# Performance work log

Hardware: AMD Instinct MI355X
Metric: run time of the kernel (lower is better)

The kernel has to match this reference:

```python
import jax, jax.numpy as jnp
import numpy as np
from jax import lax

# db4 analysis filters (pywt convention)
DEC_LO = np.array([-0.010597401785069032, 0.0328830116668852, 0.030841381835560764,
                   -0.18703481171909309, -0.027983769416859854, 0.6308807679298589,
                   0.7148465705529157, 0.2303778133088965], dtype=np.float32)
DEC_HI = np.array([-0.2303778133088965, 0.7148465705529157, -0.6308807679298589,
                   -0.027983769416859854, 0.18703481171909309, 0.030841381835560764,
                   -0.0328830116668852, -0.010597401785069032], dtype=np.float32)
LF = 8          # db4 filter length
J = 4           # wavelet levels
H = 768         # hidden size per modality
B, S = 8, 2048  # batch, seq len

# pytorch_wavelets cross-correlates with time-reversed dec filters (afb)
H0R = jnp.asarray(DEC_LO[::-1].copy())
H1R = jnp.asarray(DEC_HI[::-1].copy())
# conv_transpose(rec) == cross-correlation with flip(rec); flip(rec)=dec
G0F = jnp.asarray(DEC_LO)
G1F = jnp.asarray(DEC_HI)


def afb1d(x):
    """One analysis level along last axis, zero-pad mode. x: (B, C, N)."""
    b, c, n = x.shape
    outsize = (n + LF - 1) // 2          # pywt.dwt_coeff_len, mode='zero'
    p = 2 * (outsize - 1) - n + LF       # total pad (extra goes on the right)
    kern = jnp.stack([H0R, H1R])[:, None, :]               # (2,1,LF)
    y = lax.conv_general_dilated(x.reshape(b * c, 1, n), kern,
                                 (2,), [(p // 2, p - p // 2)])
    return y[:, 0].reshape(b, c, outsize), y[:, 1].reshape(b, c, outsize)


def sfb1d(lo, hi):
    """One synthesis level (inverse of afb1d). lo, hi: (B, C, N)."""
    b, c, n = lo.shape
    z = jnp.stack([lo.reshape(b * c, n), hi.reshape(b * c, n)], axis=1)  # (BC,2,N)
    kern = jnp.stack([G0F, G1F])[None]                     # (1,2,LF)
    # conv_transpose(stride=2, padding=LF-2) as lhs-dilated cross-correlation
    y = lax.conv_general_dilated(z, kern, (1,), [(1, 1)], lhs_dilation=(2,))
    return y[:, 0].reshape(b, c, 2 * n - LF + 2)


def dwt1d(x):
    highs = []
    lo = x
    for _ in range(J):
        lo, hi = afb1d(lo)
        highs.append(hi)
    return lo, highs


def idwt1d(lo, highs):
    for hi in highs[::-1]:
        if lo.shape[-1] > hi.shape[-1]:   # static shape check (as in IDWT1D)
            lo = lo[..., :-1]
        lo = sfb1d(lo, hi)
    return lo


def setup_inputs() -> dict:
    key = jax.random.key(0)
    k1, k2, k3 = jax.random.split(key, 3)
    x = jax.random.normal(k1, (B, S, 3 * H), dtype=jnp.float32)
    low_w = jax.random.normal(k2, (3, 3, H, H), dtype=jnp.float32) * 0.02
    high_w = jax.random.normal(k3, (3, J, 3, H, H), dtype=jnp.float32) * 0.02
    weight = jnp.ones((3,), dtype=jnp.float32)   # config['initializer_weight']
    return {"x": x, "low_w": low_w, "high_w": high_w, "weight": weight}


def reference(x, low_w, high_w, weight):
    b, s, _ = x.shape
    xs = jnp.stack(jnp.split(x, 3, axis=-1))               # (3,B,S,H) modalities
    xt = xs.transpose(0, 1, 3, 2).reshape(3 * b, H, s)     # DWT along seq axis
    lo, highs = dwt1d(xt)
    lo_s = lo.reshape(3, b, H, -1).transpose(0, 1, 3, 2)           # (3,B,Nl,H)
    hi_s = [h.reshape(3, b, H, -1).transpose(0, 1, 3, 2) for h in highs]

    # cross-modal sigmoid-gated fusion: m = target modal, j = source modal
    g = jnp.einsum('jbnh,mjgh->mjbng', lo_s, low_w)
    fused_l = (jax.nn.sigmoid(g) * lo_s[None]).sum(axis=1)         # (3,B,Nl,H)
    fused_h = []
    for k in range(J):
        gk = jnp.einsum('jbnh,mjgh->mjbng', hi_s[k], high_w[:, k])
        fused_h.append((jax.nn.sigmoid(gk) * hi_s[k][None]).sum(axis=1))

    fl = fused_l.transpose(0, 1, 3, 2).reshape(3 * b, H, -1)
    fh = [f.transpose(0, 1, 3, 2).reshape(3 * b, H, -1) for f in fused_h]
    recon = idwt1d(fl, fh).reshape(3, b, H, s).transpose(0, 1, 3, 2)  # (3,B,S,H)
    return (recon - xs) * weight[:, None, None, None]
```

## Files before the change

kernel.cpp:

```cpp
#include <hip/hip_runtime.h>
#include <hip/hip_bf16.h>

#define H 768
#define NB 8
#define SLEN 2048
#define N1 1027
#define N2 517
#define N3 262
#define N4 134

typedef short bf16x8 __attribute__((ext_vector_type(8)));
typedef float f32x4 __attribute__((ext_vector_type(4)));
typedef unsigned short ushortx4 __attribute__((ext_vector_type(4)));
typedef unsigned short ushortx8 __attribute__((ext_vector_type(8)));

__device__ __forceinline__ float sigmoidf(float v) {
    return 1.0f / (1.0f + __expf(-v));
}

__device__ __forceinline__ unsigned short f2bf(float f) {
    union { float f; unsigned u; } v; v.f = f;
    unsigned r = v.u + 0x7fffu + ((v.u >> 16) & 1u);
    return (unsigned short)(r >> 16);
}

__device__ __forceinline__ float bf2f(unsigned short u) {
    union { unsigned u; float f; } v; v.u = ((unsigned)u) << 16;
    return v.f;
}

__device__ __forceinline__ void gload_lds16(const void* g, void* l) {
    __builtin_amdgcn_global_load_lds(
        (const __attribute__((address_space(1))) unsigned int*)g,
        (__attribute__((address_space(3))) unsigned int*)l,
        16, 0, 0);
}

__global__ __launch_bounds__(192)
void dwt_analysis_kernel(const float* __restrict__ in,
                         float* __restrict__ lo_f32,
                         unsigned short* __restrict__ lo_bf,
                         unsigned short* __restrict__ hi_bf,
                         int n_in, int n_out, int rows_pad,
                         long j_stride, long b_stride, long t_stride)
{
    const float h0r[8] = { 0.2303778133088965f,  0.7148465705529157f,  0.6308807679298589f,
                          -0.027983769416859854f, -0.18703481171909309f, 0.030841381835560764f,
                           0.0328830116668852f, -0.010597401785069032f };
    const float h1r[8] = { -0.010597401785069032f, -0.0328830116668852f, 0.030841381835560764f,
                            0.18703481171909309f, -0.027983769416859854f, -0.6308807679298589f,
                            0.7148465705529157f, -0.2303778133088965f };
    const int tbase = blockIdx.x * 16;
    const int jb = blockIdx.y;
    const int j = jb >> 3, b = jb & 7;
    const int h = threadIdx.x * 4;
    const float* src = in + j * j_stride + b * b_stride + h;
    const float4 z4 = make_float4(0.f, 0.f, 0.f, 0.f);

    float4 w[8];
#pragma unroll
    for (int k = 0; k < 8; ++k) {
        int s = 2 * tbase - 6 + k;
        w[k] = (s >= 0 && s < n_in) ? *(const float4*)(src + (long)s * t_stride) : z4;
    }
#pragma unroll
    for (int tt = 0; tt < 16; ++tt) {
        const int t = tbase + tt;
        if (t < n_out) {
            float lx = 0.f, ly = 0.f, lz = 0.f, lw = 0.f;
            float hx = 0.f, hy = 0.f, hz = 0.f, hw = 0.f;
#pragma unroll
            for (int k = 0; k < 8; ++k) {
                float4 v = w[(2 * tt + k) & 7];
                lx += v.x * h0r[k]; ly += v.y * h0r[k]; lz += v.z * h0r[k]; lw += v.w * h0r[k];
                hx += v.x * h1r[k]; hy += v.y * h1r[k]; hz += v.z * h1r[k]; hw += v.w * h1r[k];
            }
            const long prow = (long)j * rows_pad + b * n_out + t;
            if (lo_f32) {
                float4 o; o.x = lx; o.y = ly; o.z = lz; o.w = lw;
                *(float4*)(lo_f32 + ((long)jb * n_out + t) * H + h) = o;
            }
            if (lo_bf) {
                ushortx4 p; p[0] = f2bf(lx); p[1] = f2bf(ly); p[2] = f2bf(lz); p[3] = f2bf(lw);
                *(ushortx4*)(lo_bf + prow * H + h) = p;
            }
            ushortx4 qv; qv[0] = f2bf(hx); qv[1] = f2bf(hy); qv[2] = f2bf(hz); qv[3] = f2bf(hw);
            *(ushortx4*)(hi_bf + prow * H + h) = qv;
        }
        if (tt < 15) {
            int s0n = 2 * t + 2;
            w[(2 * tt) & 7]     = (s0n     < n_in) ? *(const float4*)(src + (long)s0n * t_stride)       : z4;
            w[(2 * tt + 1) & 7] = (s0n + 1 < n_in) ? *(const float4*)(src + (long)(s0n + 1) * t_stride) : z4;
        }
    }
}

__device__ __forceinline__ void synth_pair(const float4* wl, const float4* wh, int u,
                                           float4* oe, float4* oo)
{
    const float g0[8] = { -0.010597401785069032f, 0.0328830116668852f, 0.030841381835560764f,
                          -0.18703481171909309f, -0.027983769416859854f, 0.6308807679298589f,
                           0.7148465705529157f, 0.2303778133088965f };
    const float g1[8] = { -0.2303778133088965f, 0.7148465705529157f, -0.6308807679298589f,
                          -0.027983769416859854f, 0.18703481171909309f, 0.030841381835560764f,
                          -0.0328830116668852f, -0.010597401785069032f };
    float ex = 0.f, ey = 0.f, ez = 0.f, ew = 0.f;
    float ox = 0.f, oy = 0.f, oz = 0.f, ow = 0.f;
#pragma unroll
    for (int d = 0; d < 4; ++d) {
        float4 vl = wl[(u + d) & 3];
        float4 vh = wh[(u + d) & 3];
        const float cle = g0[2 * d + 1], che = g1[2 * d + 1];
        const float clo = g0[2 * d],     cho = g1[2 * d];
        ex += vl.x * cle + vh.x * che; ey += vl.y * cle + vh.y * che;
        ez += vl.z * cle + vh.z * che; ew += vl.w * cle + vh.w * che;
        ox += vl.x * clo + vh.x * cho; oy += vl.y * clo + vh.y * cho;
        oz += vl.z * clo + vh.z * cho; ow += vl.w * clo + vh.w * cho;
    }
    oe->x = ex; oe->y = ey; oe->z = ez; oe->w = ew;
    oo->x = ox; oo->y = oy; oo->z = oz; oo->w = ow;
}

__global__ __launch_bounds__(192)
void dwt_synth_kernel(const float* __restrict__ lo,
                      const float* __restrict__ hi,
                      float* __restrict__ out,
                      int n, int lo_alloc, int n_out)
{
    const int ubase = blockIdx.x * 16;
    const int mb = blockIdx.y;
    const int h = threadIdx.x * 4;
    const float* lop = lo + (long)mb * lo_alloc * H + h;
    const float* hip_ = hi + (long)mb * n * H + h;
    float* outp = out + (long)mb * n_out * H + h;
    const float4 z4 = make_float4(0.f, 0.f, 0.f, 0.f);

    float4 wl[4], wh[4];
#pragma unroll
    for (int d = 0; d < 4; ++d) {
        int i = ubase + d;
        bool ok = (i < n);
        wl[(ubase + d) & 3] = ok ? *(const float4*)(lop + (long)i * H) : z4;
        wh[(ubase + d) & 3] = ok ? *(const float4*)(hip_ + (long)i * H) : z4;
    }
#pragma unroll
    for (int uu = 0; uu < 16; ++uu) {
        const int u = ubase + uu;
        if (2 * u < n_out) {
            float4 oe, oo;
            synth_pair(wl, wh, u, &oe, &oo);
            *(float4*)(outp + (long)(2 * u) * H) = oe;
            *(float4*)(outp + (long)(2 * u + 1) * H) = oo;
        }
        if (uu < 15) {
            int i = u + 4;
            bool ok = (i < n);
            wl[u & 3] = ok ? *(const float4*)(lop + (long)i * H) : z4;
            wh[u & 3] = ok ? *(const float4*)(hip_ + (long)i * H) : z4;
        }
    }
}

__global__ __launch_bounds__(192)
void dwt_synth_final_kernel(const float* __restrict__ lo,
                            const float* __restrict__ hi,
                            const float* __restrict__ x,
                            const float* __restrict__ weight,
                            float* __restrict__ out,
                            int n, int lo_alloc)
{
    const int ubase = blockIdx.x * 16;
    const int mb = blockIdx.y;
    const int m = mb >> 3, b = mb & 7;
    const int h = threadIdx.x * 4;
    const float* lop = lo + (long)mb * lo_alloc * H + h;
    const float* hip_ = hi + (long)mb * n * H + h;
    const float* xp = x + ((long)b * SLEN) * 2304 + (long)m * H + h;
    float* outp = out + (long)mb * SLEN * H + h;
    const float wgt = weight[m];
    const float4 z4 = make_float4(0.f, 0.f, 0.f, 0.f);

    float4 wl[4], wh[4];
#pragma unroll
    for (int d = 0; d < 4; ++d) {
        int i = ubase + d;
        bool ok = (i < n);
        wl[(ubase + d) & 3] = ok ? *(const float4*)(lop + (long)i * H) : z4;
        wh[(ubase + d) & 3] = ok ? *(const float4*)(hip_ + (long)i * H) : z4;
    }
#pragma unroll
    for (int uu = 0; uu < 16; ++uu) {
        const int u = ubase + uu;
        {
            float4 oe, oo;
            synth_pair(wl, wh, u, &oe, &oo);
            float4 xe = *(const float4*)(xp + (long)(2 * u) * 2304);
            float4 xo = *(const float4*)(xp + (long)(2 * u + 1) * 2304);
            float4 re, ro;
            re.x = (oe.x - xe.x) * wgt; re.y = (oe.y - xe.y) * wgt;
            re.z = (oe.z - xe.z) * wgt; re.w = (oe.w - xe.w) * wgt;
            ro.x = (oo.x - xo.x) * wgt; ro.y = (oo.y - xo.y) * wgt;
            ro.z = (oo.z - xo.z) * wgt; ro.w = (oo.w - xo.w) * wgt;
            *(float4*)(outp + (long)(2 * u) * H) = re;
            *(float4*)(outp + (long)(2 * u + 1) * H) = ro;
        }
        if (uu < 15) {
            int i = u + 4;
            bool ok = (i < n);
            wl[u & 3] = ok ? *(const float4*)(lop + (long)i * H) : z4;
            wh[u & 3] = ok ? *(const float4*)(hip_ + (long)i * H) : z4;
        }
    }
}

__global__ __launch_bounds__(256)
void cvt_weights_kernel(const float* __restrict__ low_w,
                        const float* __restrict__ high_w,
                        unsigned short* __restrict__ Wl,
                        unsigned short* __restrict__ Wh)
{
    const long HH = (long)H * H;
    const long nlow8 = 9L * HH / 8;
    const long total8 = 45L * HH / 8;
    long stride = (long)gridDim.x * blockDim.x;
    for (long idx = (long)blockIdx.x * blockDim.x + threadIdx.x; idx < total8; idx += stride) {
        const float* src;
        unsigned short* dst;
        if (idx < nlow8) { long e = idx * 8; src = low_w + e; dst = Wl + e; }
        else             { long e = (idx - nlow8) * 8; src = high_w + e; dst = Wh + e; }
        float4 a = *(const float4*)src;
        float4 b = *(const float4*)(src + 4);
        ushortx8 o;
        o[0] = f2bf(a.x); o[1] = f2bf(a.y); o[2] = f2bf(a.z); o[3] = f2bf(a.w);
        o[4] = f2bf(b.x); o[5] = f2bf(b.y); o[6] = f2bf(b.z); o[7] = f2bf(b.w);
        *(ushortx8*)dst = o;
    }
}

#define A1OFF 0L
#define A2OFF 19169280L
#define A3OFF 28901376L
#define A4OFF 33914880L
#define ALOFF 36569088L
#define WLOFF 39223296L
#define WHOFF 44531712L
#define F1OFF 0L
#define F2OFF 18929664L
#define F3OFF 28459008L
#define F4OFF 33288192L
#define FLOFF 35758080L
#define HHL (768L * 768L)

__global__ __launch_bounds__(512, 4)
void gating_mfma_kernel(const unsigned short* __restrict__ R2,
                        float* __restrict__ F0)
{
    __shared__ unsigned short ldsA[2][2][128 * 32];
    __shared__ unsigned short ldsB[2][2][128 * 32];
    const int tid = threadIdx.x;
    const int lane = tid & 63;
    const int wid = tid >> 6;
    const int wr = wid >> 2;
    const int wc = wid & 3;
    const int kq = lane >> 4;
    const int lr = lane & 15;

    const int nwg = 2394;
    const int orig = blockIdx.x;
    const int q = nwg >> 3, rm = nwg & 7;
    const int xcd = orig & 7, bidx = orig >> 3;
    const int swz = (xcd < rm) ? (xcd * (q + 1) + bidx)
                               : (rm * (q + 1) + (xcd - rm) * q + bidx);
    const int rt = swz / 18;
    const int ct = swz - rt * 18;
    const int m = ct / 6;
    const int gBlk = ct - m * 6;

    int rtl, rowsReal, rowsPad; long aOff, fOff, wOff, wm;
    if (rt < 65)       { rtl = rt;       rowsReal = 8216; rowsPad = 8320; aOff = A1OFF; fOff = F1OFF; wOff = WHOFF + 0 * 3 * HHL; wm = 12 * HHL; }
    else if (rt < 98)  { rtl = rt - 65;  rowsReal = 4136; rowsPad = 4224; aOff = A2OFF; fOff = F2OFF; wOff = WHOFF + 1 * 3 * HHL; wm = 12 * HHL; }
    else if (rt < 115) { rtl = rt - 98;  rowsReal = 2096; rowsPad = 2176; aOff = A3OFF; fOff = F3OFF; wOff = WHOFF + 2 * 3 * HHL; wm = 12 * HHL; }
    else if (rt < 124) { rtl = rt - 115; rowsReal = 1072; rowsPad = 1152; aOff = A4OFF; fOff = F4OFF; wOff = WHOFF + 3 * 3 * HHL; wm = 12 * HHL; }
    else               { rtl = rt - 124; rowsReal = 1072; rowsPad = 1152; aOff = ALOFF; fOff = FLOFF; wOff = WLOFF;              wm = 3 * HHL; }
    const int rowLocal = rtl * 128;

    const int gcol = gBlk * 128 + wc * 32;
    const int k0_g = gcol & ~63;
    const int kh_g = wc & 1;

    const int srow = wid * 16 + (lane >> 2);
    const int scol = 8 * ((lane & 3) ^ ((lane >> 3) & 3));

    const int sl = kq ^ ((lr >> 1) & 3);

    const unsigned short* Ag[3];
    const unsigned short* Wg[3];
    const unsigned short* Wb = R2 + wOff + (long)m * wm;
#pragma unroll
    for (int j = 0; j < 3; ++j) {
        Ag[j] = R2 + aOff + (long)j * rowsPad * H + (long)(rowLocal + srow) * H + scol;
        Wg[j] = Wb + (long)j * HHL + (long)(gBlk * 128 + srow) * H + scol;
    }

    f32x4 fus[4][2], acc[4][2];
    unsigned gp[4][2][2];
#pragma unroll
    for (int a = 0; a < 4; ++a)
#pragma unroll
        for (int b = 0; b < 2; ++b) { fus[a][b] = (f32x4)0.f; acc[a][b] = (f32x4)0.f; }

#define STAGE(buf, jj, kk) do {                                              \
    gload_lds16(Ag[jj] + (kk),      (char*)&ldsA[buf][0][0] + wid * 1024);   \
    gload_lds16(Ag[jj] + (kk) + 32, (char*)&ldsA[buf][1][0] + wid * 1024);   \
    gload_lds16(Wg[jj] + (kk),      (char*)&ldsB[buf][0][0] + wid * 1024);   \
    gload_lds16(Wg[jj] + (kk) + 32, (char*)&ldsB[buf][1][0] + wid * 1024);   \
} while (0)

    STAGE(0, 0, 0);
    STAGE(1, 0, 64);

#pragma unroll
    for (int t = 0; t < 36; ++t) {
        const int cur = t & 1;
        const int j = t / 12;
        const int kk0 = (t - j * 12) * 64;

        if (t < 35) asm volatile("s_waitcnt vmcnt(4)" ::: "memory");
        else        asm volatile("s_waitcnt vmcnt(0)" ::: "memory");
        __builtin_amdgcn_s_barrier();

        if (kk0 == k0_g) {
            const unsigned short* gsrc = kh_g ? &ldsA[cur][1][0] : &ldsA[cur][0][0];
#pragma unroll
            for (int mi = 0; mi < 4; ++mi)
#pragma unroll
                for (int ni = 0; ni < 2; ++ni)
#pragma unroll
                    for (int rp = 0; rp < 2; ++rp) {
                        const int rl = wr * 64 + mi * 16 + kq * 4 + rp * 2;
                        const int ec = ni * 16 + lr;
                        const int slotg = (ec >> 3) ^ ((kq * 2 + rp) & 3);
                        const int eoff = slotg * 8 + (ec & 7);
                        unsigned a0 = gsrc[rl * 32 + eoff];
                        unsigned a1 = gsrc[(rl + 1) * 32 + eoff];
                        gp[mi][ni][rp] = a0 | (a1 << 16);
                    }
        }

#pragma unroll
        for (int kh = 0; kh < 2; ++kh) {
            bf16x8 af[4], bfr[2];
#pragma unroll
            for (int mi = 0; mi < 4; ++mi)
                af[mi] = *(const bf16x8*)&ldsA[cur][kh][(wr * 64 + mi * 16 + lr) * 32 + sl * 8];
#pragma unroll
            for (int ni = 0; ni < 2; ++ni)
                bfr[ni] = *(const bf16x8*)&ldsB[cur][kh][(wc * 32 + ni * 16 + lr) * 32 + sl * 8];
#pragma unroll
            for (int mi = 0; mi < 4; ++mi)
#pragma unroll
                for (int ni = 0; ni < 2; ++ni)
                    acc[mi][ni] = __builtin_amdgcn_mfma_f32_16x16x32_bf16(
                        af[mi], bfr[ni], acc[mi][ni], 0, 0, 0);
        }

        if (t - j * 12 == 11) {
#pragma unroll
            for (int mi = 0; mi < 4; ++mi)
#pragma unroll
                for (int ni = 0; ni < 2; ++ni) {
#pragma unroll
                    for (int rp = 0; rp < 2; ++rp) {
                        float c0 = bf2f((unsigned short)(gp[mi][ni][rp] & 0xffffu));
                        float c1 = bf2f((unsigned short)(gp[mi][ni][rp] >> 16));
                        fus[mi][ni][rp * 2]     += sigmoidf(acc[mi][ni][rp * 2])     * c0;
                        fus[mi][ni][rp * 2 + 1] += sigmoidf(acc[mi][ni][rp * 2 + 1]) * c1;
                    }
                    acc[mi][ni] = (f32x4)0.f;
                }
        }

        asm volatile("" ::: "memory");
        __builtin_amdgcn_s_barrier();
        asm volatile("" ::: "memory");
        if (t < 34) {
            const int tp = t + 2;
            const int jp = tp / 12;
            STAGE(cur, jp, (tp - jp * 12) * 64);
        }
    }
#undef STAGE

    float* F = F0 + fOff;
#pragma unroll
    for (int mi = 0; mi < 4; ++mi)
#pragma unroll
        for (int ni = 0; ni < 2; ++ni)
#pragma unroll
            for (int reg = 0; reg < 4; ++reg) {
                const int rl = wr * 64 + mi * 16 + kq * 4 + reg;
                const int r = rowLocal + rl;
                if (r < rowsReal) {
                    const int g = gBlk * 128 + wc * 32 + ni * 16 + lr;
                    F[((long)m * rowsReal + r) * H + g] = fus[mi][ni][reg];
                }
            }
}

static inline int grid_for(long total) {
    long g = (total + 255) / 256;
    if (g > 16384) g = 16384;
    return (int)g;
}

extern "C" void kernel_launch(void* const* d_in, const int* in_sizes, int n_in,
                              void* d_out, int out_size, void* d_ws, size_t ws_size,
                              hipStream_t stream)
{
    const float* x      = (const float*)d_in[0];
    const float* low_w  = (const float*)d_in[1];
    const float* high_w = (const float*)d_in[2];
    const float* weight = (const float*)d_in[3];
    float* out = (float*)d_out;
    float* ws  = (float*)d_ws;

    const long HH = (long)H * H;
    const int rows1p = 8320, rows2p = 4224, rows3p = 2176, rows4p = 1152;

    float* B_lo1 = ws;
    float* B_lo2 = B_lo1 + 24L * N1 * H;
    float* B_lo3 = B_lo2 + 24L * N2 * H;
    float* F_hi1 = ws + F1OFF;
    float* F_hi2 = ws + F2OFF;
    float* F_hi3 = ws + F3OFF;
    float* F_hi4 = ws + F4OFF;
    float* F_lo  = ws + FLOFF;

    const long SZF = 24L * (N1 + N2 + N3 + 2 * N4) * H;
    float* R2f = ws + SZF;
    unsigned short* R2 = (unsigned short*)R2f;
    unsigned short* Abf1 = R2 + A1OFF;
    unsigned short* Abf2 = R2 + A2OFF;
    unsigned short* Abf3 = R2 + A3OFF;
    unsigned short* Abf4 = R2 + A4OFF;
    unsigned short* AbfL = R2 + ALOFF;
    unsigned short* Wl   = R2 + WLOFF;
    unsigned short* Wh   = R2 + WHOFF;
    float* Y1 = R2f;
    float* Y2 = Y1 + 24L * 262 * H;
    float* Y3 = Y2 + 24L * 518 * H;

    hipLaunchKernelGGL(dwt_analysis_kernel, dim3((N1 + 15) / 16, 24), dim3(192), 0, stream,
                       x, B_lo1, (unsigned short*)nullptr, Abf1,
                       SLEN, N1, rows1p, 768L, (long)SLEN * 2304, 2304L);
    hipLaunchKernelGGL(dwt_analysis_kernel, dim3((N2 + 15) / 16, 24), dim3(192), 0, stream,
                       B_lo1, B_lo2, (unsigned short*)nullptr, Abf2,
                       N1, N2, rows2p, 8L * N1 * H, (long)N1 * H, (long)H);
    hipLaunchKernelGGL(dwt_analysis_kernel, dim3((N3 + 15) / 16, 24), dim3(192), 0, stream,
                       B_lo2, B_lo3, (unsigned short*)nullptr, Abf3,
                       N2, N3, rows3p, 8L * N2 * H, (long)N2 * H, (long)H);
    hipLaunchKernelGGL(dwt_analysis_kernel, dim3((N4 + 15) / 16, 24), dim3(192), 0, stream,
                       B_lo3, (float*)nullptr, AbfL, Abf4,
                       N3, N4, rows4p, 8L * N3 * H, (long)N3 * H, (long)H);

    hipLaunchKernelGGL(cvt_weights_kernel, dim3(grid_for(45L * HH / 8)), dim3(256), 0, stream,
                       low_w, high_w, Wl, Wh);

    hipLaunchKernelGGL(gating_mfma_kernel, dim3(2394), dim3(512), 0, stream, R2, ws);

    hipLaunchKernelGGL(dwt_synth_kernel, dim3(9, 24), dim3(192), 0, stream,
                       F_lo, F_hi4, Y1, N4, N4, 262);
    hipLaunchKernelGGL(dwt_synth_kernel, dim3(17, 24), dim3(192), 0, stream,
                       Y1, F_hi3, Y2, N3, 262, 518);
    hipLaunchKernelGGL(dwt_synth_kernel, dim3(33, 24), dim3(192), 0, stream,
                       Y2, F_hi2, Y3, N2, 518, 1028);
    hipLaunchKernelGGL(dwt_synth_final_kernel, dim3(64, 24), dim3(192), 0, stream,
                       Y3, F_hi1, x, weight, out, N1, 1028);
}
```

Measured before the change: 601.1 us.

## Widen gating GEMM tile to 128x256 and raise MFMA wave priority

The gating GEMM tile grows from 128x128 to 128x256 output columns per workgroup. The grid halves, and each wave now computes a 64x64 sub-tile with 16 accumulators, which doubles the reuse of each A fragment loaded from LDS and cuts redundant A traffic from global memory. The gate-value extraction is remapped so each wave reads the diagonal K tile that matches its own columns. s_setprio is placed around the MFMA block. In exchange the kernel uses more registers and LDS, and launch bounds drop to 2 waves per SIMD, so occupancy and latency hiding are lower.

```diff
diff --git a/kernel.cpp b/kernel.cpp
--- a/kernel.cpp
+++ b/kernel.cpp
@@ -251,12 +251,12 @@
 #define FLOFF 35758080L
 #define HHL (768L * 768L)
 
-__global__ __launch_bounds__(512, 4)
+__global__ __launch_bounds__(512, 2)
 void gating_mfma_kernel(const unsigned short* __restrict__ R2,
                         float* __restrict__ F0)
 {
     __shared__ unsigned short ldsA[2][2][128 * 32];
-    __shared__ unsigned short ldsB[2][2][128 * 32];
+    __shared__ unsigned short ldsB[2][2][256 * 32];
     const int tid = threadIdx.x;
     const int lane = tid & 63;
     const int wid = tid >> 6;
@@ -265,16 +265,16 @@
     const int kq = lane >> 4;
     const int lr = lane & 15;
 
-    const int nwg = 2394;
+    const int nwg = 1197;
     const int orig = blockIdx.x;
     const int q = nwg >> 3, rm = nwg & 7;
     const int xcd = orig & 7, bidx = orig >> 3;
     const int swz = (xcd < rm) ? (xcd * (q + 1) + bidx)
                                : (rm * (q + 1) + (xcd - rm) * q + bidx);
-    const int rt = swz / 18;
-    const int ct = swz - rt * 18;
-    const int m = ct / 6;
-    const int gBlk = ct - m * 6;
+    const int rt = swz / 9;
+    const int ct = swz - rt * 9;
+    const int m = ct / 3;
+    const int colTile = ct - m * 3;
 
     int rtl, rowsReal, rowsPad; long aOff, fOff, wOff, wm;
     if (rt < 65)       { rtl = rt;       rowsReal = 8216; rowsPad = 8320; aOff = A1OFF; fOff = F1OFF; wOff = WHOFF + 0 * 3 * HHL; wm = 12 * HHL; }
@@ -283,37 +283,40 @@
     else if (rt < 124) { rtl = rt - 115; rowsReal = 1072; rowsPad = 1152; aOff = A4OFF; fOff = F4OFF; wOff = WHOFF + 3 * 3 * HHL; wm = 12 * HHL; }
     else               { rtl = rt - 124; rowsReal = 1072; rowsPad = 1152; aOff = ALOFF; fOff = FLOFF; wOff = WLOFF;              wm = 3 * HHL; }
     const int rowLocal = rtl * 128;
-
-    const int gcol = gBlk * 128 + wc * 32;
-    const int k0_g = gcol & ~63;
-    const int kh_g = wc & 1;
-
-    const int srow = wid * 16 + (lane >> 2);
+    const int colBase = colTile * 256;
+
+    const int ctw = colTile * 4 + wc;
+
+    const int srow = (lane >> 2);
     const int scol = 8 * ((lane & 3) ^ ((lane >> 3) & 3));
 
     const int sl = kq ^ ((lr >> 1) & 3);
 
     const unsigned short* Ag[3];
-    const unsigned short* Wg[3];
+    const unsigned short* Wg0[3];
+    const unsigned short* Wg1[3];
     const unsigned short* Wb = R2 + wOff + (long)m * wm;
 #pragma unroll
     for (int j = 0; j < 3; ++j) {
-        Ag[j] = R2 + aOff + (long)j * rowsPad * H + (long)(rowLocal + srow) * H + scol;
-        Wg[j] = Wb + (long)j * HHL + (long)(gBlk * 128 + srow) * H + scol;
-    }
-
-    f32x4 fus[4][2], acc[4][2];
-    unsigned gp[4][2][2];
+        Ag[j]  = R2 + aOff + (long)j * rowsPad * H + (long)(rowLocal + wid * 16 + srow) * H + scol;
+        Wg0[j] = Wb + (long)j * HHL + (long)(colBase + wid * 16 + srow) * H + scol;
+        Wg1[j] = Wb + (long)j * HHL + (long)(colBase + 128 + wid * 16 + srow) * H + scol;
+    }
+
+    f32x4 fus[4][4], acc[4][4];
+    unsigned gp[4][4][2];
 #pragma unroll
     for (int a = 0; a < 4; ++a)
 #pragma unroll
-        for (int b = 0; b < 2; ++b) { fus[a][b] = (f32x4)0.f; acc[a][b] = (f32x4)0.f; }
-
-#define STAGE(buf, jj, kk) do {                                              \
-    gload_lds16(Ag[jj] + (kk),      (char*)&ldsA[buf][0][0] + wid * 1024);   \
-    gload_lds16(Ag[jj] + (kk) + 32, (char*)&ldsA[buf][1][0] + wid * 1024);   \
-    gload_lds16(Wg[jj] + (kk),      (char*)&ldsB[buf][0][0] + wid * 1024);   \
-    gload_lds16(Wg[jj] + (kk) + 32, (char*)&ldsB[buf][1][0] + wid * 1024);   \
+        for (int b = 0; b < 4; ++b) { fus[a][b] = (f32x4)0.f; acc[a][b] = (f32x4)0.f; }
+
+#define STAGE(buf, jj, kk) do {                                                    \
+    gload_lds16(Ag[jj] + (kk),       (char*)&ldsA[buf][0][0] + wid * 1024);        \
+    gload_lds16(Ag[jj] + (kk) + 32,  (char*)&ldsA[buf][1][0] + wid * 1024);        \
+    gload_lds16(Wg0[jj] + (kk),      (char*)&ldsB[buf][0][0] + wid * 1024);        \
+    gload_lds16(Wg1[jj] + (kk),      (char*)&ldsB[buf][0][0] + (8 + wid) * 1024);  \
+    gload_lds16(Wg0[jj] + (kk) + 32, (char*)&ldsB[buf][1][0] + wid * 1024);        \
+    gload_lds16(Wg1[jj] + (kk) + 32, (char*)&ldsB[buf][1][0] + (8 + wid) * 1024);  \
 } while (0)
 
     STAGE(0, 0, 0);
@@ -323,52 +326,56 @@
     for (int t = 0; t < 36; ++t) {
         const int cur = t & 1;
         const int j = t / 12;
-        const int kk0 = (t - j * 12) * 64;
-
-        if (t < 35) asm volatile("s_waitcnt vmcnt(4)" ::: "memory");
+        const int kt = t - j * 12;
+
+        if (t < 35) asm volatile("s_waitcnt vmcnt(6)" ::: "memory");
         else        asm volatile("s_waitcnt vmcnt(0)" ::: "memory");
         __builtin_amdgcn_s_barrier();
 
-        if (kk0 == k0_g) {
-            const unsigned short* gsrc = kh_g ? &ldsA[cur][1][0] : &ldsA[cur][0][0];
+        if (kt == ctw) {
 #pragma unroll
             for (int mi = 0; mi < 4; ++mi)
 #pragma unroll
-                for (int ni = 0; ni < 2; ++ni)
+                for (int ni = 0; ni < 4; ++ni) {
+                    const int khg = ni >> 1;
+                    const int ec32 = (ni & 1) * 16 + lr;
+                    const unsigned short* gsrc = &ldsA[cur][khg][0];
 #pragma unroll
                     for (int rp = 0; rp < 2; ++rp) {
                         const int rl = wr * 64 + mi * 16 + kq * 4 + rp * 2;
-                        const int ec = ni * 16 + lr;
-                        const int slotg = (ec >> 3) ^ ((kq * 2 + rp) & 3);
-                        const int eoff = slotg * 8 + (ec & 7);
+                        const int slotg = (ec32 >> 3) ^ ((kq * 2 + rp) & 3);
+                        const int eoff = slotg * 8 + (ec32 & 7);
                         unsigned a0 = gsrc[rl * 32 + eoff];
                         unsigned a1 = gsrc[(rl + 1) * 32 + eoff];
                         gp[mi][ni][rp] = a0 | (a1 << 16);
                     }
+                }
         }
 
 #pragma unroll
         for (int kh = 0; kh < 2; ++kh) {
-            bf16x8 af[4], bfr[2];
+            bf16x8 af[4], bfr[4];
 #pragma unroll
             for (int mi = 0; mi < 4; ++mi)
                 af[mi] = *(const bf16x8*)&ldsA[cur][kh][(wr * 64 + mi * 16 + lr) * 32 + sl * 8];
 #pragma unroll
-            for (int ni = 0; ni < 2; ++ni)
-                bfr[ni] = *(const bf16x8*)&ldsB[cur][kh][(wc * 32 + ni * 16 + lr) * 32 + sl * 8];
+            for (int ni = 0; ni < 4; ++ni)
+                bfr[ni] = *(const bf16x8*)&ldsB[cur][kh][(wc * 64 + ni * 16 + lr) * 32 + sl * 8];
+            __builtin_amdgcn_s_setprio(1);
 #pragma unroll
             for (int mi = 0; mi < 4; ++mi)
 #pragma unroll
-                for (int ni = 0; ni < 2; ++ni)
+                for (int ni = 0; ni < 4; ++ni)
                     acc[mi][ni] = __builtin_amdgcn_mfma_f32_16x16x32_bf16(
                         af[mi], bfr[ni], acc[mi][ni], 0, 0, 0);
-        }
-
-        if (t - j * 12 == 11) {
+            __builtin_amdgcn_s_setprio(0);
+        }
+
+        if (kt == 11) {
 #pragma unroll
             for (int mi = 0; mi < 4; ++mi)
 #pragma unroll
-                for (int ni = 0; ni < 2; ++ni) {
+                for (int ni = 0; ni < 4; ++ni) {
 #pragma unroll
                     for (int rp = 0; rp < 2; ++rp) {
                         float c0 = bf2f((unsigned short)(gp[mi][ni][rp] & 0xffffu));
@@ -395,13 +402,13 @@
 #pragma unroll
     for (int mi = 0; mi < 4; ++mi)
 #pragma unroll
-        for (int ni = 0; ni < 2; ++ni)
+        for (int ni = 0; ni < 4; ++ni)
 #pragma unroll
             for (int reg = 0; reg < 4; ++reg) {
                 const int rl = wr * 64 + mi * 16 + kq * 4 + reg;
                 const int r = rowLocal + rl;
                 if (r < rowsReal) {
-                    const int g = gBlk * 128 + wc * 32 + ni * 16 + lr;
+                    const int g = colBase + wc * 64 + ni * 16 + lr;
                     F[((long)m * rowsReal + r) * H + g] = fus[mi][ni][reg];
                 }
             }
@@ -466,7 +473,7 @@
     hipLaunchKernelGGL(cvt_weights_kernel, dim3(grid_for(45L * HH / 8)), dim3(256), 0, stream,
                        low_w, high_w, Wl, Wh);
 
-    hipLaunchKernelGGL(gating_mfma_kernel, dim3(2394), dim3(512), 0, stream, R2, ws);
+    hipLaunchKernelGGL(gating_mfma_kernel, dim3(1197), dim3(512), 0, stream, R2, ws);
 
     hipLaunchKernelGGL(dwt_synth_kernel, dim3(9, 24), dim3(192), 0, stream,
                        F_lo, F_hi4, Y1, N4, N4, 262);
```

Result: slower. 677.2 us (+12.7%).

## Store intermediate lowpass and large fused highpass buffers in bf16

Applied to the files above, without the earlier changes.

The analysis levels now write their lowpass output only as bf16, into the padded gating-operand layout, and the next level reads it from there instead of a separate fp32 copy. The gating kernel writes fused highpass levels 1 and 2, the two largest, as bf16, and the matching synthesis kernels are templated to convert on load. This removes one fp32 store stream per analysis level and halves the traffic of the biggest fused buffers. The cost is more rounding in the cascaded lowpass and the reconstructed highs, which may move the output further from the reference.

```diff
diff --git a/kernel.cpp b/kernel.cpp
--- a/kernel.cpp
+++ b/kernel.cpp
@@ -36,9 +36,16 @@
         16, 0, 0);
 }
 
+__device__ __forceinline__ float4 ld4(const float* p) { return *(const float4*)p; }
+__device__ __forceinline__ float4 ld4(const unsigned short* p) {
+    ushortx4 v = *(const ushortx4*)p;
+    float4 o; o.x = bf2f(v[0]); o.y = bf2f(v[1]); o.z = bf2f(v[2]); o.w = bf2f(v[3]);
+    return o;
+}
+
+template<typename InT>
 __global__ __launch_bounds__(192)
-void dwt_analysis_kernel(const float* __restrict__ in,
-                         float* __restrict__ lo_f32,
+void dwt_analysis_kernel(const InT* __restrict__ in,
                          unsigned short* __restrict__ lo_bf,
                          unsigned short* __restrict__ hi_bf,
                          int n_in, int n_out, int rows_pad,
@@ -54,14 +61,14 @@
     const int jb = blockIdx.y;
     const int j = jb >> 3, b = jb & 7;
     const int h = threadIdx.x * 4;
-    const float* src = in + j * j_stride + b * b_stride + h;
+    const InT* src = in + j * j_stride + b * b_stride + h;
     const float4 z4 = make_float4(0.f, 0.f, 0.f, 0.f);
 
     float4 w[8];
 #pragma unroll
     for (int k = 0; k < 8; ++k) {
         int s = 2 * tbase - 6 + k;
-        w[k] = (s >= 0 && s < n_in) ? *(const float4*)(src + (long)s * t_stride) : z4;
+        w[k] = (s >= 0 && s < n_in) ? ld4(src + (long)s * t_stride) : z4;
     }
 #pragma unroll
     for (int tt = 0; tt < 16; ++tt) {
@@ -76,25 +83,20 @@
                 hx += v.x * h1r[k]; hy += v.y * h1r[k]; hz += v.z * h1r[k]; hw += v.w * h1r[k];
             }
             const long prow = (long)j * rows_pad + b * n_out + t;
-            if (lo_f32) {
-                float4 o; o.x = lx; o.y = ly; o.z = lz; o.w = lw;
-                *(float4*)(lo_f32 + ((long)jb * n_out + t) * H + h) = o;
-            }
-            if (lo_bf) {
-                ushortx4 p; p[0] = f2bf(lx); p[1] = f2bf(ly); p[2] = f2bf(lz); p[3] = f2bf(lw);
-                *(ushortx4*)(lo_bf + prow * H + h) = p;
-            }
+            ushortx4 p; p[0] = f2bf(lx); p[1] = f2bf(ly); p[2] = f2bf(lz); p[3] = f2bf(lw);
+            *(ushortx4*)(lo_bf + prow * H + h) = p;
             ushortx4 qv; qv[0] = f2bf(hx); qv[1] = f2bf(hy); qv[2] = f2bf(hz); qv[3] = f2bf(hw);
             *(ushortx4*)(hi_bf + prow * H + h) = qv;
         }
         if (tt < 15) {
             int s0n = 2 * t + 2;
-            w[(2 * tt) & 7]     = (s0n     < n_in) ? *(const float4*)(src + (long)s0n * t_stride)       : z4;
-            w[(2 * tt + 1) & 7] = (s0n + 1 < n_in) ? *(const float4*)(src + (long)(s0n + 1) * t_stride) : z4;
-        }
-    }
-}
-
+            w[(2 * tt) & 7]     = (s0n     < n_in) ? ld4(src + (long)s0n * t_stride)       : z4;
+            w[(2 * tt + 1) & 7] = (s0n + 1 < n_in) ? ld4(src + (long)(s0n + 1) * t_stride) : z4;
+        }
+    }
+}
+
+template<typename HiT>
 __device__ __forceinline__ void synth_pair(const float4* wl, const float4* wh, int u,
                                            float4* oe, float4* oo)
 {
@@ -121,9 +123,10 @@
     oo->x = ox; oo->y = oy; oo->z = oz; oo->w = ow;
 }
 
+template<typename HiT>
 __global__ __launch_bounds__(192)
 void dwt_synth_kernel(const float* __restrict__ lo,
-                      const float* __restrict__ hi,
+                      const HiT* __restrict__ hi,
                       float* __restrict__ out,
                       int n, int lo_alloc, int n_out)
 {
@@ -131,7 +134,7 @@
     const int mb = blockIdx.y;
     const int h = threadIdx.x * 4;
     const float* lop = lo + (long)mb * lo_alloc * H + h;
-    const float* hip_ = hi + (long)mb * n * H + h;
+    const HiT* hip_ = hi + (long)mb * n * H + h;
     float* outp = out + (long)mb * n_out * H + h;
     const float4 z4 = make_float4(0.f, 0.f, 0.f, 0.f);
 
@@ -140,30 +143,31 @@
     for (int d = 0; d < 4; ++d) {
         int i = ubase + d;
         bool ok = (i < n);
-        wl[(ubase + d) & 3] = ok ? *(const float4*)(lop + (long)i * H) : z4;
-        wh[(ubase + d) & 3] = ok ? *(const float4*)(hip_ + (long)i * H) : z4;
+        wl[(ubase + d) & 3] = ok ? ld4(lop + (long)i * H) : z4;
+        wh[(ubase + d) & 3] = ok ? ld4(hip_ + (long)i * H) : z4;
     }
 #pragma unroll
     for (int uu = 0; uu < 16; ++uu) {
         const int u = ubase + uu;
         if (2 * u < n_out) {
             float4 oe, oo;
-            synth_pair(wl, wh, u, &oe, &oo);
+            synth_pair<HiT>(wl, wh, u, &oe, &oo);
             *(float4*)(outp + (long)(2 * u) * H) = oe;
             *(float4*)(outp + (long)(2 * u + 1) * H) = oo;
         }
         if (uu < 15) {
             int i = u + 4;
             bool ok = (i < n);
-            wl[u & 3] = ok ? *(const float4*)(lop + (long)i * H) : z4;
-            wh[u & 3] = ok ? *(const float4*)(hip_ + (long)i * H) : z4;
-        }
-    }
-}
-
+            wl[u & 3] = ok ? ld4(lop + (long)i * H) : z4;
+            wh[u & 3] = ok ? ld4(hip_ + (long)i * H) : z4;
+        }
+    }
+}
+
+template<typename HiT>
 __global__ __launch_bounds__(192)
 void dwt_synth_final_kernel(const float* __restrict__ lo,
-                            const float* __restrict__ hi,
+                            const HiT* __restrict__ hi,
                             const float* __restrict__ x,
                             const float* __restrict__ weight,
                             float* __restrict__ out,
@@ -174,7 +178,7 @@
     const int m = mb >> 3, b = mb & 7;
     const int h = threadIdx.x * 4;
     const float* lop = lo + (long)mb * lo_alloc * H + h;
-    const float* hip_ = hi + (long)mb * n * H + h;
+    const HiT* hip_ = hi + (long)mb * n * H + h;
     const float* xp = x + ((long)b * SLEN) * 2304 + (long)m * H + h;
     float* outp = out + (long)mb * SLEN * H + h;
     const float wgt = weight[m];
@@ -185,15 +189,15 @@
     for (int d = 0; d < 4; ++d) {
         int i = ubase + d;
         bool ok = (i < n);
-        wl[(ubase + d) & 3] = ok ? *(const float4*)(lop + (long)i * H) : z4;
-        wh[(ubase + d) & 3] = ok ? *(const float4*)(hip_ + (long)i * H) : z4;
+        wl[(ubase + d) & 3] = ok ? ld4(lop + (long)i * H) : z4;
+        wh[(ubase + d) & 3] = ok ? ld4(hip_ + (long)i * H) : z4;
     }
 #pragma unroll
     for (int uu = 0; uu < 16; ++uu) {
         const int u = ubase + uu;
         {
             float4 oe, oo;
-            synth_pair(wl, wh, u, &oe, &oo);
+            synth_pair<HiT>(wl, wh, u, &oe, &oo);
             float4 xe = *(const float4*)(xp + (long)(2 * u) * 2304);
             float4 xo = *(const float4*)(xp + (long)(2 * u + 1) * 2304);
             float4 re, ro;
@@ -207,8 +211,8 @@
         if (uu < 15) {
             int i = u + 4;
             bool ok = (i < n);
-            wl[u & 3] = ok ? *(const float4*)(lop + (long)i * H) : z4;
-            wh[u & 3] = ok ? *(const float4*)(hip_ + (long)i * H) : z4;
+            wl[u & 3] = ok ? ld4(lop + (long)i * H) : z4;
+            wh[u & 3] = ok ? ld4(hip_ + (long)i * H) : z4;
         }
     }
 }
@@ -276,12 +280,12 @@
     const int m = ct / 6;
     const int gBlk = ct - m * 6;
 
-    int rtl, rowsReal, rowsPad; long aOff, fOff, wOff, wm;
-    if (rt < 65)       { rtl = rt;       rowsReal = 8216; rowsPad = 8320; aOff = A1OFF; fOff = F1OFF; wOff = WHOFF + 0 * 3 * HHL; wm = 12 * HHL; }
-    else if (rt < 98)  { rtl = rt - 65;  rowsReal = 4136; rowsPad = 4224; aOff = A2OFF; fOff = F2OFF; wOff = WHOFF + 1 * 3 * HHL; wm = 12 * HHL; }
-    else if (rt < 115) { rtl = rt - 98;  rowsReal = 2096; rowsPad = 2176; aOff = A3OFF; fOff = F3OFF; wOff = WHOFF + 2 * 3 * HHL; wm = 12 * HHL; }
-    else if (rt < 124) { rtl = rt - 115; rowsReal = 1072; rowsPad = 1152; aOff = A4OFF; fOff = F4OFF; wOff = WHOFF + 3 * 3 * HHL; wm = 12 * HHL; }
-    else               { rtl = rt - 124; rowsReal = 1072; rowsPad = 1152; aOff = ALOFF; fOff = FLOFF; wOff = WLOFF;              wm = 3 * HHL; }
+    int rtl, rowsReal, rowsPad, hiBf; long aOff, fOff, wOff, wm;
+    if (rt < 65)       { rtl = rt;       rowsReal = 8216; rowsPad = 8320; aOff = A1OFF; fOff = F1OFF; wOff = WHOFF + 0 * 3 * HHL; wm = 12 * HHL; hiBf = 1; }
+    else if (rt < 98)  { rtl = rt - 65;  rowsReal = 4136; rowsPad = 4224; aOff = A2OFF; fOff = F2OFF; wOff = WHOFF + 1 * 3 * HHL; wm = 12 * HHL; hiBf = 1; }
+    else if (rt < 115) { rtl = rt - 98;  rowsReal = 2096; rowsPad = 2176; aOff = A3OFF; fOff = F3OFF; wOff = WHOFF + 2 * 3 * HHL; wm = 12 * HHL; hiBf = 0; }
+    else if (rt < 124) { rtl = rt - 115; rowsReal = 1072; rowsPad = 1152; aOff = A4OFF; fOff = F4OFF; wOff = WHOFF + 3 * 3 * HHL; wm = 12 * HHL; hiBf = 0; }
+    else               { rtl = rt - 124; rowsReal = 1072; rowsPad = 1152; aOff = ALOFF; fOff = FLOFF; wOff = WLOFF;              wm = 3 * HHL; hiBf = 0; }
     const int rowLocal = rtl * 128;
 
     const int gcol = gBlk * 128 + wc * 32;
@@ -391,20 +395,37 @@
     }
 #undef STAGE
 
-    float* F = F0 + fOff;
-#pragma unroll
-    for (int mi = 0; mi < 4; ++mi)
-#pragma unroll
-        for (int ni = 0; ni < 2; ++ni)
-#pragma unroll
-            for (int reg = 0; reg < 4; ++reg) {
-                const int rl = wr * 64 + mi * 16 + kq * 4 + reg;
-                const int r = rowLocal + rl;
-                if (r < rowsReal) {
-                    const int g = gBlk * 128 + wc * 32 + ni * 16 + lr;
-                    F[((long)m * rowsReal + r) * H + g] = fus[mi][ni][reg];
+    if (hiBf) {
+        unsigned short* Fb = (unsigned short*)(F0 + fOff);
+#pragma unroll
+        for (int mi = 0; mi < 4; ++mi)
+#pragma unroll
+            for (int ni = 0; ni < 2; ++ni)
+#pragma unroll
+                for (int reg = 0; reg < 4; ++reg) {
+                    const int rl = wr * 64 + mi * 16 + kq * 4 + reg;
+                    const int r = rowLocal + rl;
+                    if (r < rowsReal) {
+                        const int g = gBlk * 128 + wc * 32 + ni * 16 + lr;
+                        Fb[((long)m * rowsReal + r) * H + g] = f2bf(fus[mi][ni][reg]);
+                    }
                 }
-            }
+    } else {
+        float* F = F0 + fOff;
+#pragma unroll
+        for (int mi = 0; mi < 4; ++mi)
+#pragma unroll
+            for (int ni = 0; ni < 2; ++ni)
+#pragma unroll
+                for (int reg = 0; reg < 4; ++reg) {
+                    const int rl = wr * 64 + mi * 16 + kq * 4 + reg;
+                    const int r = rowLocal + rl;
+                    if (r < rowsReal) {
+                        const int g = gBlk * 128 + wc * 32 + ni * 16 + lr;
+                        F[((long)m * rowsReal + r) * H + g] = fus[mi][ni][reg];
+                    }
+                }
+    }
 }
 
 static inline int grid_for(long total) {
@@ -427,11 +448,11 @@
     const long HH = (long)H * H;
     const int rows1p = 8320, rows2p = 4224, rows3p = 2176, rows4p = 1152;
 
-    float* B_lo1 = ws;
-    float* B_lo2 = B_lo1 + 24L * N1 * H;
-    float* B_lo3 = B_lo2 + 24L * N2 * H;
-    float* F_hi1 = ws + F1OFF;
-    float* F_hi2 = ws + F2OFF;
+    unsigned short* Blo1 = (unsigned short*)ws;
+    unsigned short* Blo2 = Blo1 + 3L * rows1p * H;
+    unsigned short* Blo3 = Blo2 + 3L * rows2p * H;
+    unsigned short* F_hi1b = (unsigned short*)(ws + F1OFF);
+    unsigned short* F_hi2b = (unsigned short*)(ws + F2OFF);
     float* F_hi3 = ws + F3OFF;
     float* F_hi4 = ws + F4OFF;
     float* F_lo  = ws + FLOFF;
@@ -450,30 +471,30 @@
     float* Y2 = Y1 + 24L * 262 * H;
     float* Y3 = Y2 + 24L * 518 * H;
 
-    hipLaunchKernelGGL(dwt_analysis_kernel, dim3((N1 + 15) / 16, 24), dim3(192), 0, stream,
-                       x, B_lo1, (unsigned short*)nullptr, Abf1,
+    hipLaunchKernelGGL((dwt_analysis_kernel<float>), dim3((N1 + 15) / 16, 24), dim3(192), 0, stream,
+                       x, Blo1, Abf1,
                        SLEN, N1, rows1p, 768L, (long)SLEN * 2304, 2304L);
-    hipLaunchKernelGGL(dwt_analysis_kernel, dim3((N2 + 15) / 16, 24), dim3(192), 0, stream,
-                       B_lo1, B_lo2, (unsigned short*)nullptr, Abf2,
-                       N1, N2, rows2p, 8L * N1 * H, (long)N1 * H, (long)H);
-    hipLaunchKernelGGL(dwt_analysis_kernel, dim3((N3 + 15) / 16, 24), dim3(192), 0, stream,
-                       B_lo2, B_lo3, (unsigned short*)nullptr, Abf3,
-                       N2, N3, rows3p, 8L * N2 * H, (long)N2 * H, (long)H);
-    hipLaunchKernelGGL(dwt_analysis_kernel, dim3((N4 + 15) / 16, 24), dim3(192), 0, stream,
-                       B_lo3, (float*)nullptr, AbfL, Abf4,
-                       N3, N4, rows4p, 8L * N3 * H, (long)N3 * H, (long)H);
+    hipLaunchKernelGGL((dwt_analysis_kernel<unsigned short>), dim3((N2 + 15) / 16, 24), dim3(192), 0, stream,
+                       Blo1, Blo2, Abf2,
+                       N1, N2, rows2p, (long)rows1p * H, (long)N1 * H, (long)H);
+    hipLaunchKernelGGL((dwt_analysis_kernel<unsigned short>), dim3((N3 + 15) / 16, 24), dim3(192), 0, stream,
+                       Blo2, Blo3, Abf3,
+                       N2, N3, rows3p, (long)rows2p * H, (long)N2 * H, (long)H);
+    hipLaunchKernelGGL((dwt_analysis_kernel<unsigned short>), dim3((N4 + 15) / 16, 24), dim3(192), 0, stream,
+                       Blo3, AbfL, Abf4,
+                       N3, N4, rows4p, (long)rows3p * H, (long)N3 * H, (long)H);
 
     hipLaunchKernelGGL(cvt_weights_kernel, dim3(grid_for(45L * HH / 8)), dim3(256), 0, stream,
                        low_w, high_w, Wl, Wh);
 
     hipLaunchKernelGGL(gating_mfma_kernel, dim3(2394), dim3(512), 0, stream, R2, ws);
 
-    hipLaunchKernelGGL(dwt_synth_kernel, dim3(9, 24), dim3(192), 0, stream,
+    hipLaunchKernelGGL((dwt_synth_kernel<float>), dim3(9, 24), dim3(192), 0, stream,
                        F_lo, F_hi4, Y1, N4, N4, 262);
-    hipLaunchKernelGGL(dwt_synth_kernel, dim3(17, 24), dim3(192), 0, stream,
+    hipLaunchKernelGGL((dwt_synth_kernel<float>), dim3(17, 24), dim3(192), 0, stream,
                        Y1, F_hi3, Y2, N3, 262, 518);
-    hipLaunchKernelGGL(dwt_synth_kernel, dim3(33, 24), dim3(192), 0, stream,
-                       Y2, F_hi2, Y3, N2, 518, 1028);
-    hipLaunchKernelGGL(dwt_synth_final_kernel, dim3(64, 24), dim3(192), 0, stream,
-                       Y3, F_hi1, x, weight, out, N1, 1028);
-}
+    hipLaunchKernelGGL((dwt_synth_kernel<unsigned short>), dim3(33, 24), dim3(192), 0, stream,
+                       Y2, F_hi2b, Y3, N2, 518, 1028);
+    hipLaunchKernelGGL((dwt_synth_final_kernel<unsigned short>), dim3(64, 24), dim3(192), 0, stream,
+                       Y3, F_hi1b, x, weight, out, N1, 1028);
+}
```

Result: no change. 602.3 us (+0.2%).
